# Kernel tuning notes

Measured on AMD Instinct MI355X. Metric: run time of the kernel, lower is better.

The kernel has to match this reference:

```python
import jax, jax.numpy as jnp
import numpy as np

B, S, D_IN, D_OUT = 8, 4096, 512, 64

def setup_inputs() -> dict:
    key = jax.random.key(0)
    k1, k2, k3, k4 = jax.random.split(key, 4)
    scale = 1.0 / np.sqrt(D_IN)
    return {
        "x": jax.random.normal(k1, (B, S, D_IN), dtype=jnp.float32),
        "W_Q": jax.random.normal(k2, (D_IN, D_OUT), dtype=jnp.float32) * scale,
        "W_K": jax.random.normal(k3, (D_IN, D_OUT), dtype=jnp.float32) * scale,
        "W_V": jax.random.normal(k4, (D_IN, D_OUT), dtype=jnp.float32) * scale,
    }

def reference(x, W_Q, W_K, W_V):
    # q,k,v: [B,S,D_OUT]
    q = jnp.einsum("bsd,de->bse", x, W_Q)
    k = jnp.einsum("bsd,de->bse", x, W_K)
    v = jnp.einsum("bsd,de->bse", x, W_V)
    d_out = k.shape[-1]
    # scores: [B,S,S], causal mask (upper triangle -> -inf)
    scores = jnp.einsum("bqe,bke->bqk", q, k)
    s = q.shape[1]
    causal = jnp.tril(jnp.ones((s, s), dtype=bool))
    scores = jnp.where(causal[None, :, :], scores, -jnp.inf)
    attn = jax.nn.softmax(scores / jnp.sqrt(jnp.asarray(d_out, scores.dtype)), axis=-1)
    # dropout p=0.0 (eval) -> identity
    return jnp.einsum("bqk,bke->bqe", attn, v)
```

## Files before the change

kernel.cpp:

```cpp
#include <hip/hip_runtime.h>
#include <hip/hip_bf16.h>

#define B_    8
#define S_    4096
#define DIN   512
#define DOUT  64
#define NROWS (B_ * S_)

typedef __attribute__((ext_vector_type(8)))  short bf16x8;
typedef __attribute__((ext_vector_type(4)))  float f32x4;
typedef __attribute__((ext_vector_type(16))) float f32x16;
typedef __attribute__((ext_vector_type(2)))  unsigned int u32x2;
typedef __attribute__((ext_vector_type(2)))  int i32x2;

typedef const __attribute__((address_space(1))) unsigned int GUI;
typedef __attribute__((address_space(3))) unsigned int LUI;

__device__ __forceinline__ unsigned short f32_to_bf16(float f) {
    union { float f; unsigned int u; } c; c.f = f;
    unsigned int r = (c.u + 0x7FFFu + ((c.u >> 16) & 1u)) >> 16;
    return (unsigned short)r;
}
__device__ __forceinline__ float bf16_to_f32(unsigned short us) {
    union { unsigned int u; float f; } c; c.u = (unsigned int)us << 16;
    return c.f;
}

__device__ __forceinline__ float fast_exp2(float x) {
#if __has_builtin(__builtin_amdgcn_exp2f)
    return __builtin_amdgcn_exp2f(x);
#else
    return exp2f(x);
#endif
}

__device__ __forceinline__ float max_xor32(float v) {
    i32x2 r = __builtin_amdgcn_permlane32_swap(__float_as_int(v), __float_as_int(v),
                                               false, false);
    return fmaxf(__int_as_float(r.x), __int_as_float(r.y));
}
__device__ __forceinline__ float sum_xor32(float v) {
    i32x2 r = __builtin_amdgcn_permlane32_swap(__float_as_int(v), __float_as_int(v),
                                               false, false);
    return __int_as_float(r.x) + __int_as_float(r.y);
}

#define LDS_READS_DONE_FENCE() do {                                   \
    asm volatile("s_waitcnt lgkmcnt(0)" ::: "memory");                \
    __builtin_amdgcn_sched_barrier(0);                                \
} while (0)

__device__ __forceinline__ int pidx_of(int tp, int j) {
    if (tp < 16) return tp - 8;
    if (tp < 24) return 8 + (tp - 16) * 2 + (j - 1);
    return 24 + (tp - 24) * 3 + (j - 1);
}

__global__ void wt_convert(const float* __restrict__ WQ,
                           const float* __restrict__ WK,
                           const float* __restrict__ WV,
                           unsigned short* __restrict__ Wt2) {
    int idx = blockIdx.x * 256 + threadIdx.x;
    if (idx >= 3 * 512 * 16) return;
    int p   = idx / 8192;
    int rem = idx - p * 8192;
    int k   = rem >> 4;
    int n0  = (rem & 15) * 4;
    const float* W = (p == 0) ? WQ : ((p == 1) ? WK : WV);
    float4 v = *(const float4*)(W + k * 64 + n0);
    const int ks = k >> 5, kl = k & 31;
    float vv[4] = {v.x, v.y, v.z, v.w};
#pragma unroll
    for (int r = 0; r < 4; ++r) {
        int n = n0 + r;
        Wt2[(size_t)((ks * 12 + p * 4 + (n >> 4)) * 512) + (n & 15) * 32 + kl] =
            f32_to_bf16(vv[r]);
    }
}

__global__ __launch_bounds__(256) void qkv_proj(const float* __restrict__ x,
                                                const unsigned short* __restrict__ Wt2,
                                                unsigned short* __restrict__ QKV) {
    __shared__ alignas(16) float          xtile[2][1024];
    __shared__ alignas(16) unsigned short btile[2][6144];

    const int tid  = threadIdx.x;
    const int lane = tid & 63;
    const int wq   = tid >> 6;
    const int c15  = lane & 15;
    const int g    = lane >> 4;
    const float* xblk = x + (size_t)blockIdx.x * 32 * DIN;

    const int rw     = (wq & 1) * 16 + c15;
    const int nfbase = (wq >> 1) * 6;

    const int xrow = wq * 8 + (lane >> 3);
    const int xsl  = (lane & 7) ^ (xrow & 7);

    auto stage = [&](int slot, int ks) {
        __builtin_amdgcn_global_load_lds((GUI*)(xblk + ks * 32 + xrow * DIN + xsl * 4),
                                         (LUI*)((char*)&xtile[slot][0] + wq * 1024), 16, 0, 0);
        const unsigned short* Bs = Wt2 + (size_t)ks * 6144;
#pragma unroll
        for (int j = 0; j < 3; ++j)
            __builtin_amdgcn_global_load_lds((GUI*)(Bs + (j * 256 + tid) * 8),
                                             (LUI*)((char*)&btile[slot][0] + j * 4096 + wq * 1024),
                                             16, 0, 0);
    };
    stage(0, 0);
    stage(1, 1);

    f32x4 acc[6] = {};

    int cur = 0;
    for (int ks = 0; ks < 16; ++ks) {
        asm volatile("s_waitcnt vmcnt(4)" ::: "memory");
        asm volatile("s_barrier" ::: "memory");

        const char* xb = (const char*)&xtile[cur][0] + rw * 128;
        f32x4 a0 = *(const f32x4*)(xb + (((2 * g)     ^ (rw & 7)) << 4));
        f32x4 a1 = *(const f32x4*)(xb + (((2 * g + 1) ^ (rw & 7)) << 4));
        union { unsigned w[4]; bf16x8 v; } af;
        asm("v_cvt_pk_bf16_f32 %0, %1, %2" : "=v"(af.w[0]) : "v"(a0[0]), "v"(a0[1]));
        asm("v_cvt_pk_bf16_f32 %0, %1, %2" : "=v"(af.w[1]) : "v"(a0[2]), "v"(a0[3]));
        asm("v_cvt_pk_bf16_f32 %0, %1, %2" : "=v"(af.w[2]) : "v"(a1[0]), "v"(a1[1]));
        asm("v_cvt_pk_bf16_f32 %0, %1, %2" : "=v"(af.w[3]) : "v"(a1[2]), "v"(a1[3]));

        const char* bb = (const char*)&btile[cur][0] + c15 * 64 + g * 16;
#pragma unroll
        for (int n = 0; n < 6; ++n) {
            bf16x8 bf = *(const bf16x8*)(bb + (nfbase + n) * 1024);
            acc[n] = __builtin_amdgcn_mfma_f32_16x16x32_bf16(af.v, bf, acc[n], 0, 0, 0);
        }

        LDS_READS_DONE_FENCE();
        asm volatile("s_barrier" ::: "memory");
        {
            int tn = ks + 2; if (tn > 15) tn = 15;
            stage(cur, tn);
        }
        cur ^= 1;
    }
    asm volatile("s_waitcnt vmcnt(0)" ::: "memory");

    const int orow0 = blockIdx.x * 32 + (wq & 1) * 16 + g * 4;
#pragma unroll
    for (int n = 0; n < 6; ++n) {
        const int nfg  = nfbase + n;
        const int p    = nfg >> 2;
        const int ncol = (nfg & 3) * 16 + c15;
        if (p < 2) {
            unsigned short* outp = QKV + (size_t)p * NROWS * DOUT;
            const float sc = (p == 0) ? 0.125f * 1.44269504089f : 1.0f;
#pragma unroll
            for (int r = 0; r < 4; ++r)
                outp[(size_t)(orow0 + r) * DOUT + ncol] = f32_to_bf16(acc[n][r] * sc);
        } else {
            const int bb2  = orow0 >> 12;
            const int srow = orow0 & 4095;
            union { unsigned short s[4]; u32x2 d; } pk;
#pragma unroll
            for (int r = 0; r < 4; ++r) pk.s[r] = f32_to_bf16(acc[n][r]);
            *(u32x2*)(QKV + (size_t)2 * NROWS * DOUT +
                      ((size_t)bb2 * DOUT + ncol) * S_ + srow) = pk.d;
        }
    }
}

__global__ __launch_bounds__(256) void attn_fwd(const unsigned short* __restrict__ QKV,
                                                float* __restrict__ out,
                                                char* __restrict__ part1,
                                                float* __restrict__ ml0) {
    __shared__ alignas(16) unsigned short k_lds[2][4096];
    __shared__ alignas(16) unsigned short v_lds[2][4096];

    const int bid = blockIdx.x;
    const int b   = bid & 7;
    const int i   = bid >> 3;
    int tp, j;
    if      (i < 8)  { tp = i;                 j = 0; }
    else if (i < 24) { tp = 8 + ((i - 8) >> 1);  j = (i - 8) & 1; }
    else if (i < 48) { tp = 16 + (i - 24) / 3;   j = (i - 24) % 3; }
    else             { tp = 24 + ((i - 48) >> 2); j = (i - 48) & 3; }
    const int qb       = tp * 128;
    const int tile_lo  = 16 * j;
    const int tile_hi  = min(16 * j + 15, 2 * tp + 1);
    const int tile_cnt = tile_hi - tile_lo + 1;

    const int tid  = threadIdx.x;
    const int lane = tid & 63;
    const int wq   = tid >> 6;
    const int q31  = lane & 31;
    const int h    = lane >> 5;
    const int swz  = q31 & 7;
    const int rb0  = q31 * 128;

    const unsigned short* Qg  = QKV + (size_t)b * S_ * DOUT;
    const unsigned short* Kg  = QKV + (size_t)NROWS * DOUT + (size_t)b * S_ * DOUT;
    const unsigned short* VTg = QKV + (size_t)2 * NROWS * DOUT + (size_t)b * DOUT * S_;

    const int qrow = qb + wq * 32 + q31;
    const unsigned short* Qr = Qg + (size_t)qrow * DOUT + 8 * h;
    bf16x8 qf[4];
#pragma unroll
    for (int s = 0; s < 4; ++s) qf[s] = *(const bf16x8*)(Qr + 16 * s);
    asm volatile("s_waitcnt vmcnt(0)" ::: "memory");

    const int i0 = wq * 128 + lane;
    const int i1 = i0 + 64;
    const int r0 = i0 >> 3, s0g = (i0 & 7) ^ (r0 & 7);
    const int r1 = i1 >> 3, s1g = (i1 & 7) ^ (r1 & 7);

    auto stage = [&](int slot, int tg) {
        const unsigned short* Kt = Kg + (size_t)tg * 64 * DOUT;
        const unsigned short* Vt = VTg + tg * 64;
        char* kbase = (char*)&k_lds[slot][0] + wq * 2048;
        char* vbase = (char*)&v_lds[slot][0] + wq * 2048;
        __builtin_amdgcn_global_load_lds((GUI*)(Kt + r0 * DOUT + s0g * 8), (LUI*)kbase, 16, 0, 0);
        __builtin_amdgcn_global_load_lds((GUI*)(Kt + r1 * DOUT + s1g * 8), (LUI*)(kbase + 1024), 16, 0, 0);
        __builtin_amdgcn_global_load_lds((GUI*)(Vt + (size_t)r0 * S_ + s0g * 8), (LUI*)vbase, 16, 0, 0);
        __builtin_amdgcn_global_load_lds((GUI*)(Vt + (size_t)r1 * S_ + s1g * 8), (LUI*)(vbase + 1024), 16, 0, 0);
    };

    stage(0, tile_lo);
    stage(1, tile_lo + (tile_cnt > 1 ? 1 : 0));

    f32x16 oacc0 = {}, oacc1 = {};
    float m_r = -3.0e38f, l_r = 0.f;

    int cur = 0;
    for (int itl = 0; itl < tile_cnt; ++itl) {
        const int tg = tile_lo + itl;
        asm volatile("s_waitcnt vmcnt(4)" ::: "memory");
        asm volatile("s_barrier" ::: "memory");

        const char* kb_ = (const char*)&k_lds[cur][0];
        const char* vb_ = (const char*)&v_lds[cur][0];

        f32x16 sA = {}, sB = {};
#pragma unroll
        for (int s = 0; s < 4; ++s) {
            const int sl = ((2 * s + h) ^ swz) << 4;
            bf16x8 ka  = *(const bf16x8*)(kb_ + rb0 + sl);
            bf16x8 kb2 = *(const bf16x8*)(kb_ + rb0 + 4096 + sl);
            sA = __builtin_amdgcn_mfma_f32_32x32x16_bf16(ka,  qf[s], sA, 0, 0, 0);
            sB = __builtin_amdgcn_mfma_f32_32x32x16_bf16(kb2, qf[s], sB, 0, 0, 0);
        }

        if (tg >= 2 * tp) {
#pragma unroll
            for (int r2 = 0; r2 < 16; ++r2) {
                const int kvg = 64 * tg + (r2 & 3) + 8 * (r2 >> 2) + 4 * h;
                if (kvg      > qrow) sA[r2] = -1.0e30f;
                if (kvg + 32 > qrow) sB[r2] = -1.0e30f;
            }
        }

        float t[16];
#pragma unroll
        for (int k2 = 0; k2 < 16; ++k2) t[k2] = fmaxf(sA[k2], sB[k2]);
#pragma unroll
        for (int st = 8; st >= 1; st >>= 1)
#pragma unroll
            for (int k2 = 0; k2 < st; ++k2) t[k2] = fmaxf(t[k2], t[k2 + st]);
        float mx = max_xor32(t[0]);
        const float mnew  = fmaxf(m_r, mx);
        const float alpha = fast_exp2(m_r - mnew);
        m_r = mnew;

#pragma unroll
        for (int k2 = 0; k2 < 16; ++k2) {
            sA[k2] = fast_exp2(sA[k2] - mnew);
            sB[k2] = fast_exp2(sB[k2] - mnew);
        }
#pragma unroll
        for (int k2 = 0; k2 < 16; ++k2) t[k2] = sA[k2] + sB[k2];
#pragma unroll
        for (int st = 8; st >= 1; st >>= 1)
#pragma unroll
            for (int k2 = 0; k2 < st; ++k2) t[k2] += t[k2 + st];
        l_r = l_r * alpha + sum_xor32(t[0]);

#pragma unroll
        for (int k2 = 0; k2 < 16; ++k2) { oacc0[k2] *= alpha; oacc1[k2] *= alpha; }

#define STEP_PV(u, Pv) do {                                                        \
        const int e0 = 2 * ((u) & 1);                                              \
        unsigned pa, pb2, pc, pd;                                                  \
        asm("v_cvt_pk_bf16_f32 %0, %1, %2" : "=v"(pa)  : "v"(Pv[4*e0+0]), "v"(Pv[4*e0+1])); \
        asm("v_cvt_pk_bf16_f32 %0, %1, %2" : "=v"(pb2) : "v"(Pv[4*e0+2]), "v"(Pv[4*e0+3])); \
        asm("v_cvt_pk_bf16_f32 %0, %1, %2" : "=v"(pc)  : "v"(Pv[4*e0+4]), "v"(Pv[4*e0+5])); \
        asm("v_cvt_pk_bf16_f32 %0, %1, %2" : "=v"(pd)  : "v"(Pv[4*e0+6]), "v"(Pv[4*e0+7])); \
        i32x2 ra = __builtin_amdgcn_permlane32_swap((int)pa,  (int)pc, false, false); \
        i32x2 rb = __builtin_amdgcn_permlane32_swap((int)pb2, (int)pd, false, false); \
        union { unsigned w[4]; bf16x8 v; } pw;                                     \
        pw.w[0] = (unsigned)ra.x; pw.w[1] = (unsigned)rb.x;                        \
        pw.w[2] = (unsigned)ra.y; pw.w[3] = (unsigned)rb.y;                        \
        const int slv = ((2 * (u) + h) ^ swz) << 4;                                \
        bf16x8 vfa = *(const bf16x8*)(vb_ + rb0 + slv);                            \
        bf16x8 vfb = *(const bf16x8*)(vb_ + rb0 + 4096 + slv);                     \
        oacc0 = __builtin_amdgcn_mfma_f32_32x32x16_bf16(vfa, pw.v, oacc0, 0, 0, 0);\
        oacc1 = __builtin_amdgcn_mfma_f32_32x32x16_bf16(vfb, pw.v, oacc1, 0, 0, 0);\
    } while (0)

        STEP_PV(0, sA); STEP_PV(1, sA); STEP_PV(2, sB); STEP_PV(3, sB);
#undef STEP_PV

        LDS_READS_DONE_FENCE();
        asm volatile("s_barrier" ::: "memory");
        {
            int tn = itl + 2; if (tn >= tile_cnt) tn = tile_cnt - 1;
            stage(cur, tile_lo + tn);
        }
        cur ^= 1;
    }

    asm volatile("s_waitcnt vmcnt(0)" ::: "memory");

    const int ql = wq * 32 + q31;
    if (j == 0 && tp < 8) {
        const float linv = 1.0f / l_r;
        float* op = out + (size_t)b * S_ * DOUT + (size_t)qrow * DOUT;
#pragma unroll
        for (int e = 0; e < 4; ++e) {
            f32x4 v0 = { oacc0[4*e+0]*linv, oacc0[4*e+1]*linv, oacc0[4*e+2]*linv, oacc0[4*e+3]*linv };
            f32x4 v1 = { oacc1[4*e+0]*linv, oacc1[4*e+1]*linv, oacc1[4*e+2]*linv, oacc1[4*e+3]*linv };
            *(f32x4*)(op + 8*e + 4*h)      = v0;
            *(f32x4*)(op + 32 + 8*e + 4*h) = v1;
        }
    } else if (j == 0) {
        float* op = out + (size_t)b * S_ * DOUT + (size_t)qrow * DOUT;
#pragma unroll
        for (int e = 0; e < 4; ++e) {
            f32x4 v0 = { oacc0[4*e+0], oacc0[4*e+1], oacc0[4*e+2], oacc0[4*e+3] };
            f32x4 v1 = { oacc1[4*e+0], oacc1[4*e+1], oacc1[4*e+2], oacc1[4*e+3] };
            *(f32x4*)(op + 8*e + 4*h)      = v0;
            *(f32x4*)(op + 32 + 8*e + 4*h) = v1;
        }
        if (h == 0) {
            float* ml = ml0 + (size_t)(b * 24 + (tp - 8)) * 256;
            ml[ql] = m_r; ml[128 + ql] = l_r;
        }
    } else {
        char* pb_ = part1 + (size_t)(b * 48 + pidx_of(tp, j)) * 17408;
        if (h == 0) {
            float* mf = (float*)pb_;
            mf[ql] = m_r; mf[128 + ql] = l_r;
        }
        unsigned short* ob = (unsigned short*)(pb_ + 1024);
#pragma unroll
        for (int e = 0; e < 4; ++e) {
            union { unsigned short s[4]; u32x2 d; } k0, k1;
#pragma unroll
            for (int c = 0; c < 4; ++c) { k0.s[c] = f32_to_bf16(oacc0[4*e+c]);
                                          k1.s[c] = f32_to_bf16(oacc1[4*e+c]); }
            *(u32x2*)(ob + (size_t)ql * 64 + 8*e + 4*h)      = k0.d;
            *(u32x2*)(ob + (size_t)ql * 64 + 32 + 8*e + 4*h) = k1.d;
        }
    }
}

template<int NC>
__device__ __forceinline__ void reduce_body(int b, int tp, int q, int d,
                                            float* __restrict__ out,
                                            const char* __restrict__ part1,
                                            const float* __restrict__ ml0) {
    float* otile = out + ((size_t)b * S_ + (size_t)tp * 128) * 64;
    const float* ml = ml0 + (size_t)(b * 24 + (tp - 8)) * 256;

    float m = ml[q], l = ml[128 + q];
    float M = m;
    float mj[NC - 1], lj[NC - 1];
    const unsigned short* obs[NC - 1];
#pragma unroll
    for (int jj = 0; jj < NC - 1; ++jj) {
        const char* pb = part1 + (size_t)(b * 48 + pidx_of(tp, jj + 1)) * 17408;
        const float* mf = (const float*)pb;
        mj[jj] = mf[q]; lj[jj] = mf[128 + q];
        obs[jj] = (const unsigned short*)(pb + 1024);
        M = fmaxf(M, mj[jj]);
    }
    const float e0 = fast_exp2(m - M);
    float L = e0 * l;
    float O = e0 * otile[(size_t)q * 64 + d];
#pragma unroll
    for (int jj = 0; jj < NC - 1; ++jj) {
        const float ej = fast_exp2(mj[jj] - M);
        L += ej * lj[jj];
        O += ej * bf16_to_f32(obs[jj][(size_t)q * 64 + d]);
    }
    otile[(size_t)q * 64 + d] = O / L;
}

__global__ __launch_bounds__(256) void attn_reduce(float* __restrict__ out,
                                                   const char* __restrict__ part1,
                                                   const float* __restrict__ ml0) {
    const int bid = blockIdx.x;
    const int sub = bid & 31;
    const int tz  = (bid >> 5) % 24;
    const int b   = bid / (32 * 24);
    const int tp  = tz + 8;
    const int q   = sub * 4 + (threadIdx.x >> 6);
    const int d   = threadIdx.x & 63;

    if (tp < 16)      reduce_body<2>(b, tp, q, d, out, part1, ml0);
    else if (tp < 24) reduce_body<3>(b, tp, q, d, out, part1, ml0);
    else              reduce_body<4>(b, tp, q, d, out, part1, ml0);
}

extern "C" void kernel_launch(void* const* d_in, const int* in_sizes, int n_in,
                              void* d_out, int out_size, void* d_ws, size_t ws_size,
                              hipStream_t stream) {
    const float* x  = (const float*)d_in[0];
    const float* WQ = (const float*)d_in[1];
    const float* WK = (const float*)d_in[2];
    const float* WV = (const float*)d_in[3];

    unsigned short* Wt2   = (unsigned short*)d_ws;
    unsigned short* QKV   = Wt2 + 192 * 512;
    char*           part1 = (char*)d_ws + 12779520;
    float*          ml0   = (float*)((char*)d_ws + 19464192);

    wt_convert<<<96, 256, 0, stream>>>(WQ, WK, WV, Wt2);
    qkv_proj<<<1024, 256, 0, stream>>>(x, Wt2, QKV);
    attn_fwd<<<640, 256, 0, stream>>>(QKV, (float*)d_out, part1, ml0);
    attn_reduce<<<6144, 256, 0, stream>>>((float*)d_out, part1, ml0);
}
```

Before: 77.09 us.

## Generalize causal split-KV chunking to templated chunk size and skip idle rescales

Replaces the hardcoded 16-tile split-KV schedule with a templated chunk size computed by a constexpr prefix sum. It launches chunk size 8 when the workspace is large enough, which raises the block count for better CU balance but creates more partials for the reduce pass. It also adds a lazy online-softmax rescale that only updates the running max and rescales accumulators when some lane's new max exceeds the old one by more than a threshold, saving exp and multiply work. The reduce kernel now covers all query tiles, with an early exit for those that need no merging, and uses runtime loops in place of unrolled templates.

```diff
diff --git a/kernel.cpp b/kernel.cpp
--- a/kernel.cpp
+++ b/kernel.cpp
@@ -50,10 +50,10 @@
     __builtin_amdgcn_sched_barrier(0);                                \
 } while (0)
 
-__device__ __forceinline__ int pidx_of(int tp, int j) {
-    if (tp < 16) return tp - 8;
-    if (tp < 24) return 8 + (tp - 16) * 2 + (j - 1);
-    return 24 + (tp - 24) * 3 + (j - 1);
+constexpr int cpbf(int C) {
+    int a = 0;
+    for (int t = 0; t < 32; ++t) a += (2 * t + 2 + C - 1) / C;
+    return a;
 }
 
 __global__ void wt_convert(const float* __restrict__ WQ,
@@ -167,25 +167,31 @@
     }
 }
 
+template<int CHUNK>
 __global__ __launch_bounds__(256) void attn_fwd(const unsigned short* __restrict__ QKV,
                                                 float* __restrict__ out,
                                                 char* __restrict__ part1,
                                                 float* __restrict__ ml0) {
+    constexpr int PPB = cpbf(CHUNK) - 32;
+
     __shared__ alignas(16) unsigned short k_lds[2][4096];
     __shared__ alignas(16) unsigned short v_lds[2][4096];
 
     const int bid = blockIdx.x;
     const int b   = bid & 7;
-    const int i   = bid >> 3;
-    int tp, j;
-    if      (i < 8)  { tp = i;                 j = 0; }
-    else if (i < 24) { tp = 8 + ((i - 8) >> 1);  j = (i - 8) & 1; }
-    else if (i < 48) { tp = 16 + (i - 24) / 3;   j = (i - 24) % 3; }
-    else             { tp = 24 + ((i - 48) >> 2); j = (i - 48) & 3; }
+    const int c   = bid >> 3;
+
+    int tp = 0, acc = 0, nck = 1;
+    for (; tp < 32; ++tp) {
+        nck = (2 * tp + 2 + CHUNK - 1) / CHUNK;
+        if (c < acc + nck) break;
+        acc += nck;
+    }
+    const int j        = c - acc;
+    const int tile_lo  = CHUNK * j;
+    const int tile_hi  = min(CHUNK * j + CHUNK - 1, 2 * tp + 1);
+    const int tile_cnt = tile_hi - tile_lo + 1;
     const int qb       = tp * 128;
-    const int tile_lo  = 16 * j;
-    const int tile_hi  = min(16 * j + 15, 2 * tp + 1);
-    const int tile_cnt = tile_hi - tile_lo + 1;
 
     const int tid  = threadIdx.x;
     const int lane = tid & 63;
@@ -223,7 +229,7 @@
     };
 
     stage(0, tile_lo);
-    stage(1, tile_lo + (tile_cnt > 1 ? 1 : 0));
+    stage(1, tile_lo + 1);
 
     f32x16 oacc0 = {}, oacc1 = {};
     float m_r = -3.0e38f, l_r = 0.f;
@@ -263,15 +269,21 @@
         for (int st = 8; st >= 1; st >>= 1)
 #pragma unroll
             for (int k2 = 0; k2 < st; ++k2) t[k2] = fmaxf(t[k2], t[k2 + st]);
-        float mx = max_xor32(t[0]);
-        const float mnew  = fmaxf(m_r, mx);
-        const float alpha = fast_exp2(m_r - mnew);
-        m_r = mnew;
+        const float mx = max_xor32(t[0]);
+
+        if (__any(mx > m_r + 11.5f)) {
+            const float mnew  = fmaxf(m_r, mx);
+            const float alpha = fast_exp2(m_r - mnew);
+            m_r = mnew;
+            l_r *= alpha;
+#pragma unroll
+            for (int k2 = 0; k2 < 16; ++k2) { oacc0[k2] *= alpha; oacc1[k2] *= alpha; }
+        }
 
 #pragma unroll
         for (int k2 = 0; k2 < 16; ++k2) {
-            sA[k2] = fast_exp2(sA[k2] - mnew);
-            sB[k2] = fast_exp2(sB[k2] - mnew);
+            sA[k2] = fast_exp2(sA[k2] - m_r);
+            sB[k2] = fast_exp2(sB[k2] - m_r);
         }
 #pragma unroll
         for (int k2 = 0; k2 < 16; ++k2) t[k2] = sA[k2] + sB[k2];
@@ -279,10 +291,7 @@
         for (int st = 8; st >= 1; st >>= 1)
 #pragma unroll
             for (int k2 = 0; k2 < st; ++k2) t[k2] += t[k2 + st];
-        l_r = l_r * alpha + sum_xor32(t[0]);
-
-#pragma unroll
-        for (int k2 = 0; k2 < 16; ++k2) { oacc0[k2] *= alpha; oacc1[k2] *= alpha; }
+        l_r += sum_xor32(t[0]);
 
 #define STEP_PV(u, Pv) do {                                                        \
         const int e0 = 2 * ((u) & 1);                                              \
@@ -318,7 +327,7 @@
     asm volatile("s_waitcnt vmcnt(0)" ::: "memory");
 
     const int ql = wq * 32 + q31;
-    if (j == 0 && tp < 8) {
+    if (nck == 1) {
         const float linv = 1.0f / l_r;
         float* op = out + (size_t)b * S_ * DOUT + (size_t)qrow * DOUT;
 #pragma unroll
@@ -338,11 +347,11 @@
             *(f32x4*)(op + 32 + 8*e + 4*h) = v1;
         }
         if (h == 0) {
-            float* ml = ml0 + (size_t)(b * 24 + (tp - 8)) * 256;
+            float* ml = ml0 + (size_t)(b * 32 + tp) * 256;
             ml[ql] = m_r; ml[128 + ql] = l_r;
         }
     } else {
-        char* pb_ = part1 + (size_t)(b * 48 + pidx_of(tp, j)) * 17408;
+        char* pb_ = part1 + (size_t)(b * PPB + (acc - tp) + (j - 1)) * 17408;
         if (h == 0) {
             float* mf = (float*)pb_;
             mf[ql] = m_r; mf[128 + ql] = l_r;
@@ -352,60 +361,53 @@
         for (int e = 0; e < 4; ++e) {
             union { unsigned short s[4]; u32x2 d; } k0, k1;
 #pragma unroll
-            for (int c = 0; c < 4; ++c) { k0.s[c] = f32_to_bf16(oacc0[4*e+c]);
-                                          k1.s[c] = f32_to_bf16(oacc1[4*e+c]); }
+            for (int cc = 0; cc < 4; ++cc) { k0.s[cc] = f32_to_bf16(oacc0[4*e+cc]);
+                                             k1.s[cc] = f32_to_bf16(oacc1[4*e+cc]); }
             *(u32x2*)(ob + (size_t)ql * 64 + 8*e + 4*h)      = k0.d;
             *(u32x2*)(ob + (size_t)ql * 64 + 32 + 8*e + 4*h) = k1.d;
         }
     }
 }
 
-template<int NC>
-__device__ __forceinline__ void reduce_body(int b, int tp, int q, int d,
-                                            float* __restrict__ out,
-                                            const char* __restrict__ part1,
-                                            const float* __restrict__ ml0) {
-    float* otile = out + ((size_t)b * S_ + (size_t)tp * 128) * 64;
-    const float* ml = ml0 + (size_t)(b * 24 + (tp - 8)) * 256;
-
-    float m = ml[q], l = ml[128 + q];
-    float M = m;
-    float mj[NC - 1], lj[NC - 1];
-    const unsigned short* obs[NC - 1];
-#pragma unroll
-    for (int jj = 0; jj < NC - 1; ++jj) {
-        const char* pb = part1 + (size_t)(b * 48 + pidx_of(tp, jj + 1)) * 17408;
-        const float* mf = (const float*)pb;
-        mj[jj] = mf[q]; lj[jj] = mf[128 + q];
-        obs[jj] = (const unsigned short*)(pb + 1024);
-        M = fmaxf(M, mj[jj]);
-    }
-    const float e0 = fast_exp2(m - M);
-    float L = e0 * l;
-    float O = e0 * otile[(size_t)q * 64 + d];
-#pragma unroll
-    for (int jj = 0; jj < NC - 1; ++jj) {
-        const float ej = fast_exp2(mj[jj] - M);
-        L += ej * lj[jj];
-        O += ej * bf16_to_f32(obs[jj][(size_t)q * 64 + d]);
-    }
-    otile[(size_t)q * 64 + d] = O / L;
-}
-
+template<int CHUNK>
 __global__ __launch_bounds__(256) void attn_reduce(float* __restrict__ out,
                                                    const char* __restrict__ part1,
                                                    const float* __restrict__ ml0) {
+    constexpr int PPB = cpbf(CHUNK) - 32;
+
     const int bid = blockIdx.x;
     const int sub = bid & 31;
-    const int tz  = (bid >> 5) % 24;
-    const int b   = bid / (32 * 24);
-    const int tp  = tz + 8;
-    const int q   = sub * 4 + (threadIdx.x >> 6);
-    const int d   = threadIdx.x & 63;
-
-    if (tp < 16)      reduce_body<2>(b, tp, q, d, out, part1, ml0);
-    else if (tp < 24) reduce_body<3>(b, tp, q, d, out, part1, ml0);
-    else              reduce_body<4>(b, tp, q, d, out, part1, ml0);
+    const int tp  = (bid >> 5) & 31;
+    const int b   = bid >> 10;
+
+    const int nck = (2 * tp + 2 + CHUNK - 1) / CHUNK;
+    if (nck < 2) return;
+    int acc = 0;
+    for (int t2 = 0; t2 < tp; ++t2) acc += (2 * t2 + 2 + CHUNK - 1) / CHUNK;
+    const int pbase = acc - tp;
+
+    const int q = sub * 4 + (threadIdx.x >> 6);
+    const int d = threadIdx.x & 63;
+
+    float* otile = out + ((size_t)b * S_ + (size_t)tp * 128) * 64;
+    const float* ml = ml0 + (size_t)(b * 32 + tp) * 256;
+
+    float M = ml[q];
+    for (int jj = 1; jj < nck; ++jj) {
+        const float* mf = (const float*)(part1 + (size_t)(b * PPB + pbase + jj - 1) * 17408);
+        M = fmaxf(M, mf[q]);
+    }
+    const float e0 = fast_exp2(ml[q] - M);
+    float L = e0 * ml[128 + q];
+    float O = e0 * otile[(size_t)q * 64 + d];
+    for (int jj = 1; jj < nck; ++jj) {
+        const char* pb = part1 + (size_t)(b * PPB + pbase + jj - 1) * 17408;
+        const float* mf = (const float*)pb;
+        const float ej = fast_exp2(mf[q] - M);
+        L += ej * mf[128 + q];
+        O += ej * bf16_to_f32(((const unsigned short*)(pb + 1024))[(size_t)q * 64 + d]);
+    }
+    otile[(size_t)q * 64 + d] = O / L;
 }
 
 extern "C" void kernel_launch(void* const* d_in, const int* in_sizes, int n_in,
@@ -419,10 +421,23 @@
     unsigned short* Wt2   = (unsigned short*)d_ws;
     unsigned short* QKV   = Wt2 + 192 * 512;
     char*           part1 = (char*)d_ws + 12779520;
-    float*          ml0   = (float*)((char*)d_ws + 19464192);
+    float* out = (float*)d_out;
 
     wt_convert<<<96, 256, 0, stream>>>(WQ, WK, WV, Wt2);
     qkv_proj<<<1024, 256, 0, stream>>>(x, Wt2, QKV);
-    attn_fwd<<<640, 256, 0, stream>>>(QKV, (float*)d_out, part1, ml0);
-    attn_reduce<<<6144, 256, 0, stream>>>((float*)d_out, part1, ml0);
-}
+
+    constexpr size_t P8  = (size_t)8 * (cpbf(8)  - 32) * 17408;
+    constexpr size_t P16 = (size_t)8 * (cpbf(16) - 32) * 17408;
+    constexpr size_t ML  = (size_t)8 * 32 * 1024;
+    const size_t need8 = 12779520 + P8 + ML;
+
+    if (ws_size >= need8) {
+        float* ml0 = (float*)(part1 + P8);
+        attn_fwd<8><<<8 * cpbf(8), 256, 0, stream>>>(QKV, out, part1, ml0);
+        attn_reduce<8><<<8192, 256, 0, stream>>>(out, part1, ml0);
+    } else {
+        float* ml0 = (float*)(part1 + P16);
+        attn_fwd<16><<<8 * cpbf(16), 256, 0, stream>>>(QKV, out, part1, ml0);
+        attn_reduce<16><<<8192, 256, 0, stream>>>(out, part1, ml0);
+    }
+}
```

After: 87.07 us. 1.13x slower.

## Rework attention to 8 waves of 16x16 MFMA with lazy rescale

Applied to the files above, without the earlier changes.

The attention kernel moves from 4 waves using 32x32x16 MFMAs (32 query rows per wave) to 8 waves using 16x16x32 MFMAs (16 query rows per wave), with 512 threads per block. Probabilities are now sent through a per-wave LDS buffer instead of permlane swaps, and the online-softmax rescale of the accumulators is skipped unless the running max grows by more than a threshold. s_setprio is also raised around the MFMA sections. The aim is more parallelism per CU and less register pressure, at the cost of extra LDS traffic and smaller MFMA shapes.

```diff
diff --git a/kernel.cpp b/kernel.cpp
--- a/kernel.cpp
+++ b/kernel.cpp
@@ -9,7 +9,6 @@
 
 typedef __attribute__((ext_vector_type(8)))  short bf16x8;
 typedef __attribute__((ext_vector_type(4)))  float f32x4;
-typedef __attribute__((ext_vector_type(16))) float f32x16;
 typedef __attribute__((ext_vector_type(2)))  unsigned int u32x2;
 typedef __attribute__((ext_vector_type(2)))  int i32x2;
 
@@ -167,18 +166,19 @@
     }
 }
 
-__global__ __launch_bounds__(256) void attn_fwd(const unsigned short* __restrict__ QKV,
+__global__ __launch_bounds__(512) void attn_fwd(const unsigned short* __restrict__ QKV,
                                                 float* __restrict__ out,
                                                 char* __restrict__ part1,
                                                 float* __restrict__ ml0) {
     __shared__ alignas(16) unsigned short k_lds[2][4096];
     __shared__ alignas(16) unsigned short v_lds[2][4096];
+    __shared__ alignas(16) unsigned short p_lds[8][1024];
 
     const int bid = blockIdx.x;
     const int b   = bid & 7;
     const int i   = bid >> 3;
     int tp, j;
-    if      (i < 8)  { tp = i;                 j = 0; }
+    if      (i < 8)  { tp = i;                   j = 0; }
     else if (i < 24) { tp = 8 + ((i - 8) >> 1);  j = (i - 8) & 1; }
     else if (i < 48) { tp = 16 + (i - 24) / 3;   j = (i - 24) % 3; }
     else             { tp = 24 + ((i - 48) >> 2); j = (i - 48) & 3; }
@@ -190,121 +190,129 @@
     const int tid  = threadIdx.x;
     const int lane = tid & 63;
     const int wq   = tid >> 6;
-    const int q31  = lane & 31;
-    const int h    = lane >> 5;
-    const int swz  = q31 & 7;
-    const int rb0  = q31 * 128;
+    const int c15  = lane & 15;
+    const int g    = lane >> 4;
 
     const unsigned short* Qg  = QKV + (size_t)b * S_ * DOUT;
     const unsigned short* Kg  = QKV + (size_t)NROWS * DOUT + (size_t)b * S_ * DOUT;
     const unsigned short* VTg = QKV + (size_t)2 * NROWS * DOUT + (size_t)b * DOUT * S_;
 
-    const int qrow = qb + wq * 32 + q31;
-    const unsigned short* Qr = Qg + (size_t)qrow * DOUT + 8 * h;
-    bf16x8 qf[4];
-#pragma unroll
-    for (int s = 0; s < 4; ++s) qf[s] = *(const bf16x8*)(Qr + 16 * s);
+    const int ql   = wq * 16 + c15;
+    const int qrow = qb + ql;
+    const size_t qoff = (size_t)qrow * DOUT;
+    bf16x8 qf0 = *(const bf16x8*)(Qg + qoff + g * 8);
+    bf16x8 qf1 = *(const bf16x8*)(Qg + qoff + 32 + g * 8);
     asm volatile("s_waitcnt vmcnt(0)" ::: "memory");
 
-    const int i0 = wq * 128 + lane;
-    const int i1 = i0 + 64;
-    const int r0 = i0 >> 3, s0g = (i0 & 7) ^ (r0 & 7);
-    const int r1 = i1 >> 3, s1g = (i1 & 7) ^ (r1 & 7);
+    const int row = tid >> 3;
+    const int sl  = (tid & 7) ^ (row & 7);
 
     auto stage = [&](int slot, int tg) {
         const unsigned short* Kt = Kg + (size_t)tg * 64 * DOUT;
         const unsigned short* Vt = VTg + tg * 64;
-        char* kbase = (char*)&k_lds[slot][0] + wq * 2048;
-        char* vbase = (char*)&v_lds[slot][0] + wq * 2048;
-        __builtin_amdgcn_global_load_lds((GUI*)(Kt + r0 * DOUT + s0g * 8), (LUI*)kbase, 16, 0, 0);
-        __builtin_amdgcn_global_load_lds((GUI*)(Kt + r1 * DOUT + s1g * 8), (LUI*)(kbase + 1024), 16, 0, 0);
-        __builtin_amdgcn_global_load_lds((GUI*)(Vt + (size_t)r0 * S_ + s0g * 8), (LUI*)vbase, 16, 0, 0);
-        __builtin_amdgcn_global_load_lds((GUI*)(Vt + (size_t)r1 * S_ + s1g * 8), (LUI*)(vbase + 1024), 16, 0, 0);
+        char* kbase = (char*)&k_lds[slot][0] + wq * 1024;
+        char* vbase = (char*)&v_lds[slot][0] + wq * 1024;
+        __builtin_amdgcn_global_load_lds((GUI*)(Kt + row * DOUT + sl * 8), (LUI*)kbase, 16, 0, 0);
+        __builtin_amdgcn_global_load_lds((GUI*)(Vt + (size_t)row * S_ + sl * 8), (LUI*)vbase, 16, 0, 0);
     };
 
     stage(0, tile_lo);
-    stage(1, tile_lo + (tile_cnt > 1 ? 1 : 0));
-
-    f32x16 oacc0 = {}, oacc1 = {};
+    stage(1, tile_lo + 1);
+
+    f32x4 oacc[4] = {};
     float m_r = -3.0e38f, l_r = 0.f;
 
     int cur = 0;
     for (int itl = 0; itl < tile_cnt; ++itl) {
         const int tg = tile_lo + itl;
-        asm volatile("s_waitcnt vmcnt(4)" ::: "memory");
+        asm volatile("s_waitcnt vmcnt(2)" ::: "memory");
         asm volatile("s_barrier" ::: "memory");
 
-        const char* kb_ = (const char*)&k_lds[cur][0];
-        const char* vb_ = (const char*)&v_lds[cur][0];
-
-        f32x16 sA = {}, sB = {};
-#pragma unroll
-        for (int s = 0; s < 4; ++s) {
-            const int sl = ((2 * s + h) ^ swz) << 4;
-            bf16x8 ka  = *(const bf16x8*)(kb_ + rb0 + sl);
-            bf16x8 kb2 = *(const bf16x8*)(kb_ + rb0 + 4096 + sl);
-            sA = __builtin_amdgcn_mfma_f32_32x32x16_bf16(ka,  qf[s], sA, 0, 0, 0);
-            sB = __builtin_amdgcn_mfma_f32_32x32x16_bf16(kb2, qf[s], sB, 0, 0, 0);
-        }
+        const char* kb = (const char*)&k_lds[cur][0];
+        const char* vb = (const char*)&v_lds[cur][0];
+
+        f32x4 s[4];
+        __builtin_amdgcn_s_setprio(1);
+#pragma unroll
+        for (int nf = 0; nf < 4; ++nf) {
+            const char* krow = kb + (nf * 16 + c15) * 128;
+            bf16x8 kf0 = *(const bf16x8*)(krow + ((g ^ (c15 & 7)) << 4));
+            bf16x8 kf1 = *(const bf16x8*)(krow + (((4 + g) ^ (c15 & 7)) << 4));
+            f32x4 z = {};
+            z = __builtin_amdgcn_mfma_f32_16x16x32_bf16(kf0, qf0, z, 0, 0, 0);
+            z = __builtin_amdgcn_mfma_f32_16x16x32_bf16(kf1, qf1, z, 0, 0, 0);
+            s[nf] = z;
+        }
+        __builtin_amdgcn_s_setprio(0);
 
         if (tg >= 2 * tp) {
 #pragma unroll
-            for (int r2 = 0; r2 < 16; ++r2) {
-                const int kvg = 64 * tg + (r2 & 3) + 8 * (r2 >> 2) + 4 * h;
-                if (kvg      > qrow) sA[r2] = -1.0e30f;
-                if (kvg + 32 > qrow) sB[r2] = -1.0e30f;
+            for (int nf = 0; nf < 4; ++nf)
+#pragma unroll
+                for (int r = 0; r < 4; ++r)
+                    if (64 * tg + 16 * nf + 4 * g + r > qrow) s[nf][r] = -1.0e30f;
+        }
+
+        float mx = s[0][0];
+#pragma unroll
+        for (int nf = 0; nf < 4; ++nf)
+#pragma unroll
+            for (int r = 0; r < 4; ++r) mx = fmaxf(mx, s[nf][r]);
+        mx = max_xor32(mx);
+        mx = fmaxf(mx, __shfl_xor(mx, 16, 64));
+
+        if (__any(mx > m_r + 11.5f)) {
+            const float mnew  = fmaxf(m_r, mx);
+            const float alpha = fast_exp2(m_r - mnew);
+            m_r = mnew;
+            l_r *= alpha;
+#pragma unroll
+            for (int df = 0; df < 4; ++df)
+#pragma unroll
+                for (int r = 0; r < 4; ++r) oacc[df][r] *= alpha;
+        }
+
+        float p[4][4];
+        float sum = 0.f;
+#pragma unroll
+        for (int nf = 0; nf < 4; ++nf)
+#pragma unroll
+            for (int r = 0; r < 4; ++r) {
+                p[nf][r] = fast_exp2(s[nf][r] - m_r);
+                sum += p[nf][r];
             }
-        }
-
-        float t[16];
-#pragma unroll
-        for (int k2 = 0; k2 < 16; ++k2) t[k2] = fmaxf(sA[k2], sB[k2]);
-#pragma unroll
-        for (int st = 8; st >= 1; st >>= 1)
-#pragma unroll
-            for (int k2 = 0; k2 < st; ++k2) t[k2] = fmaxf(t[k2], t[k2 + st]);
-        float mx = max_xor32(t[0]);
-        const float mnew  = fmaxf(m_r, mx);
-        const float alpha = fast_exp2(m_r - mnew);
-        m_r = mnew;
-
-#pragma unroll
-        for (int k2 = 0; k2 < 16; ++k2) {
-            sA[k2] = fast_exp2(sA[k2] - mnew);
-            sB[k2] = fast_exp2(sB[k2] - mnew);
-        }
-#pragma unroll
-        for (int k2 = 0; k2 < 16; ++k2) t[k2] = sA[k2] + sB[k2];
-#pragma unroll
-        for (int st = 8; st >= 1; st >>= 1)
-#pragma unroll
-            for (int k2 = 0; k2 < st; ++k2) t[k2] += t[k2 + st];
-        l_r = l_r * alpha + sum_xor32(t[0]);
-
-#pragma unroll
-        for (int k2 = 0; k2 < 16; ++k2) { oacc0[k2] *= alpha; oacc1[k2] *= alpha; }
-
-#define STEP_PV(u, Pv) do {                                                        \
-        const int e0 = 2 * ((u) & 1);                                              \
-        unsigned pa, pb2, pc, pd;                                                  \
-        asm("v_cvt_pk_bf16_f32 %0, %1, %2" : "=v"(pa)  : "v"(Pv[4*e0+0]), "v"(Pv[4*e0+1])); \
-        asm("v_cvt_pk_bf16_f32 %0, %1, %2" : "=v"(pb2) : "v"(Pv[4*e0+2]), "v"(Pv[4*e0+3])); \
-        asm("v_cvt_pk_bf16_f32 %0, %1, %2" : "=v"(pc)  : "v"(Pv[4*e0+4]), "v"(Pv[4*e0+5])); \
-        asm("v_cvt_pk_bf16_f32 %0, %1, %2" : "=v"(pd)  : "v"(Pv[4*e0+6]), "v"(Pv[4*e0+7])); \
-        i32x2 ra = __builtin_amdgcn_permlane32_swap((int)pa,  (int)pc, false, false); \
-        i32x2 rb = __builtin_amdgcn_permlane32_swap((int)pb2, (int)pd, false, false); \
-        union { unsigned w[4]; bf16x8 v; } pw;                                     \
-        pw.w[0] = (unsigned)ra.x; pw.w[1] = (unsigned)rb.x;                        \
-        pw.w[2] = (unsigned)ra.y; pw.w[3] = (unsigned)rb.y;                        \
-        const int slv = ((2 * (u) + h) ^ swz) << 4;                                \
-        bf16x8 vfa = *(const bf16x8*)(vb_ + rb0 + slv);                            \
-        bf16x8 vfb = *(const bf16x8*)(vb_ + rb0 + 4096 + slv);                     \
-        oacc0 = __builtin_amdgcn_mfma_f32_32x32x16_bf16(vfa, pw.v, oacc0, 0, 0, 0);\
-        oacc1 = __builtin_amdgcn_mfma_f32_32x32x16_bf16(vfb, pw.v, oacc1, 0, 0, 0);\
-    } while (0)
-
-        STEP_PV(0, sA); STEP_PV(1, sA); STEP_PV(2, sB); STEP_PV(3, sB);
-#undef STEP_PV
+        sum = sum_xor32(sum);
+        sum += __shfl_xor(sum, 16, 64);
+        l_r += sum;
+
+#pragma unroll
+        for (int nf = 0; nf < 4; ++nf)
+#pragma unroll
+            for (int pr = 0; pr < 2; ++pr) {
+                unsigned pw;
+                asm("v_cvt_pk_bf16_f32 %0, %1, %2"
+                    : "=v"(pw) : "v"(p[nf][2 * pr]), "v"(p[nf][2 * pr + 1]));
+                const int w = 8 * nf + 2 * g + pr;
+                *(unsigned*)((char*)&p_lds[wq][0] + c15 * 128 +
+                             (((w >> 2) ^ (c15 & 7)) << 4) + (w & 3) * 4) = pw;
+            }
+
+        bf16x8 pf[2];
+#pragma unroll
+        for (int kk = 0; kk < 2; ++kk)
+            pf[kk] = *(const bf16x8*)((char*)&p_lds[wq][0] + c15 * 128 +
+                                      (((4 * kk + g) ^ (c15 & 7)) << 4));
+
+        __builtin_amdgcn_s_setprio(1);
+#pragma unroll
+        for (int df = 0; df < 4; ++df) {
+            const char* vrow = vb + (df * 16 + c15) * 128;
+            bf16x8 vf0 = *(const bf16x8*)(vrow + ((g ^ (c15 & 7)) << 4));
+            bf16x8 vf1 = *(const bf16x8*)(vrow + (((4 + g) ^ (c15 & 7)) << 4));
+            oacc[df] = __builtin_amdgcn_mfma_f32_16x16x32_bf16(vf0, pf[0], oacc[df], 0, 0, 0);
+            oacc[df] = __builtin_amdgcn_mfma_f32_16x16x32_bf16(vf1, pf[1], oacc[df], 0, 0, 0);
+        }
+        __builtin_amdgcn_s_setprio(0);
 
         LDS_READS_DONE_FENCE();
         asm volatile("s_barrier" ::: "memory");
@@ -317,45 +325,39 @@
 
     asm volatile("s_waitcnt vmcnt(0)" ::: "memory");
 
-    const int ql = wq * 32 + q31;
     if (j == 0 && tp < 8) {
         const float linv = 1.0f / l_r;
         float* op = out + (size_t)b * S_ * DOUT + (size_t)qrow * DOUT;
 #pragma unroll
-        for (int e = 0; e < 4; ++e) {
-            f32x4 v0 = { oacc0[4*e+0]*linv, oacc0[4*e+1]*linv, oacc0[4*e+2]*linv, oacc0[4*e+3]*linv };
-            f32x4 v1 = { oacc1[4*e+0]*linv, oacc1[4*e+1]*linv, oacc1[4*e+2]*linv, oacc1[4*e+3]*linv };
-            *(f32x4*)(op + 8*e + 4*h)      = v0;
-            *(f32x4*)(op + 32 + 8*e + 4*h) = v1;
+        for (int df = 0; df < 4; ++df) {
+            f32x4 v = { oacc[df][0] * linv, oacc[df][1] * linv,
+                        oacc[df][2] * linv, oacc[df][3] * linv };
+            *(f32x4*)(op + df * 16 + 4 * g) = v;
         }
     } else if (j == 0) {
         float* op = out + (size_t)b * S_ * DOUT + (size_t)qrow * DOUT;
 #pragma unroll
-        for (int e = 0; e < 4; ++e) {
-            f32x4 v0 = { oacc0[4*e+0], oacc0[4*e+1], oacc0[4*e+2], oacc0[4*e+3] };
-            f32x4 v1 = { oacc1[4*e+0], oacc1[4*e+1], oacc1[4*e+2], oacc1[4*e+3] };
-            *(f32x4*)(op + 8*e + 4*h)      = v0;
-            *(f32x4*)(op + 32 + 8*e + 4*h) = v1;
-        }
-        if (h == 0) {
+        for (int df = 0; df < 4; ++df) {
+            f32x4 v = { oacc[df][0], oacc[df][1], oacc[df][2], oacc[df][3] };
+            *(f32x4*)(op + df * 16 + 4 * g) = v;
+        }
+        if (g == 0) {
             float* ml = ml0 + (size_t)(b * 24 + (tp - 8)) * 256;
             ml[ql] = m_r; ml[128 + ql] = l_r;
         }
     } else {
         char* pb_ = part1 + (size_t)(b * 48 + pidx_of(tp, j)) * 17408;
-        if (h == 0) {
+        if (g == 0) {
             float* mf = (float*)pb_;
             mf[ql] = m_r; mf[128 + ql] = l_r;
         }
         unsigned short* ob = (unsigned short*)(pb_ + 1024);
 #pragma unroll
-        for (int e = 0; e < 4; ++e) {
-            union { unsigned short s[4]; u32x2 d; } k0, k1;
-#pragma unroll
-            for (int c = 0; c < 4; ++c) { k0.s[c] = f32_to_bf16(oacc0[4*e+c]);
-                                          k1.s[c] = f32_to_bf16(oacc1[4*e+c]); }
-            *(u32x2*)(ob + (size_t)ql * 64 + 8*e + 4*h)      = k0.d;
-            *(u32x2*)(ob + (size_t)ql * 64 + 32 + 8*e + 4*h) = k1.d;
+        for (int df = 0; df < 4; ++df) {
+            union { unsigned short s2[4]; u32x2 d; } pk;
+#pragma unroll
+            for (int r = 0; r < 4; ++r) pk.s2[r] = f32_to_bf16(oacc[df][r]);
+            *(u32x2*)(ob + (size_t)ql * 64 + df * 16 + 4 * g) = pk.d;
         }
     }
 }
@@ -423,6 +425,6 @@
 
     wt_convert<<<96, 256, 0, stream>>>(WQ, WK, WV, Wt2);
     qkv_proj<<<1024, 256, 0, stream>>>(x, Wt2, QKV);
-    attn_fwd<<<640, 256, 0, stream>>>(QKV, (float*)d_out, part1, ml0);
+    attn_fwd<<<640, 512, 0, stream>>>(QKV, (float*)d_out, part1, ml0);
     attn_reduce<<<6144, 256, 0, stream>>>((float*)d_out, part1, ml0);
 }
```

After: 71.19 us. -7.6%, faster.

## Replace online softmax max with Cauchy-Schwarz bound from Q and K norms

Applied to the files above, without the earlier changes.

Adds two small kernels that compute per-query norms and a running prefix max of per-tile key norms. The attention kernel then uses |q|·max|k| as a fixed softmax offset instead of tracking a running max, which removes the per-tile max reduction, rescaling of the accumulators and the cross-lane max swap. The split-KV reduce no longer needs exponent rescaling, and block order is reversed so the longer tiles launch first. The bound can sit far above the true max, so exp2 values may underflow and lose precision or give a zero denominator on other input distributions, and the two extra launches add overhead.

```diff
diff --git a/kernel.cpp b/kernel.cpp
--- a/kernel.cpp
+++ b/kernel.cpp
@@ -34,11 +34,6 @@
 #endif
 }
 
-__device__ __forceinline__ float max_xor32(float v) {
-    i32x2 r = __builtin_amdgcn_permlane32_swap(__float_as_int(v), __float_as_int(v),
-                                               false, false);
-    return fmaxf(__int_as_float(r.x), __int_as_float(r.y));
-}
 __device__ __forceinline__ float sum_xor32(float v) {
     i32x2 r = __builtin_amdgcn_permlane32_swap(__float_as_int(v), __float_as_int(v),
                                                false, false);
@@ -55,6 +50,8 @@
     if (tp < 24) return 8 + (tp - 16) * 2 + (j - 1);
     return 24 + (tp - 24) * 3 + (j - 1);
 }
+
+#define PART_STRIDE 16896
 
 __global__ void wt_convert(const float* __restrict__ WQ,
                            const float* __restrict__ WK,
@@ -167,7 +164,59 @@
     }
 }
 
+__global__ __launch_bounds__(512) void qk_norms(const unsigned short* __restrict__ QKV,
+                                                float* __restrict__ qn,
+                                                float* __restrict__ ktm) {
+    __shared__ float lds[64];
+    const int bid  = blockIdx.x;
+    const bool isK = bid >= 512;
+    const int blk  = isK ? bid - 512 : bid;
+    const int tid  = threadIdx.x;
+    const int rowl = tid >> 3;
+    const int part = tid & 7;
+    const size_t row = (size_t)blk * 64 + rowl;
+
+    const unsigned short* src = QKV + (isK ? (size_t)NROWS * DOUT : 0) +
+                                row * DOUT + part * 8;
+    bf16x8 v = *(const bf16x8*)src;
+    float s = 0.f;
+#pragma unroll
+    for (int i2 = 0; i2 < 8; ++i2) {
+        float f = bf16_to_f32((unsigned short)v[i2]);
+        s += f * f;
+    }
+    s += __shfl_xor(s, 1, 64);
+    s += __shfl_xor(s, 2, 64);
+    s += __shfl_xor(s, 4, 64);
+
+    if (!isK) {
+        if (part == 0) qn[row] = sqrtf(s);
+    } else {
+        if (part == 0) lds[rowl] = s;
+        __syncthreads();
+        if (tid < 64) {
+            float m = lds[tid];
+#pragma unroll
+            for (int st = 32; st >= 1; st >>= 1)
+                m = fmaxf(m, __shfl_xor(m, st, 64));
+            if (tid == 0) ktm[blk] = sqrtf(m);
+        }
+    }
+}
+
+__global__ void kpref(const float* __restrict__ ktm, float* __restrict__ pm) {
+    const int b = threadIdx.x;
+    if (b >= 8) return;
+    float m = 0.f;
+    for (int t = 0; t < 64; ++t) {
+        m = fmaxf(m, ktm[b * 64 + t]);
+        pm[b * 64 + t] = m;
+    }
+}
+
 __global__ __launch_bounds__(256) void attn_fwd(const unsigned short* __restrict__ QKV,
+                                                const float* __restrict__ qn,
+                                                const float* __restrict__ pm,
                                                 float* __restrict__ out,
                                                 char* __restrict__ part1,
                                                 float* __restrict__ ml0) {
@@ -176,9 +225,9 @@
 
     const int bid = blockIdx.x;
     const int b   = bid & 7;
-    const int i   = bid >> 3;
+    const int i   = 79 - (bid >> 3);
     int tp, j;
-    if      (i < 8)  { tp = i;                 j = 0; }
+    if      (i < 8)  { tp = i;                   j = 0; }
     else if (i < 24) { tp = 8 + ((i - 8) >> 1);  j = (i - 8) & 1; }
     else if (i < 48) { tp = 16 + (i - 24) / 3;   j = (i - 24) % 3; }
     else             { tp = 24 + ((i - 48) >> 2); j = (i - 48) & 3; }
@@ -204,6 +253,8 @@
     bf16x8 qf[4];
 #pragma unroll
     for (int s = 0; s < 4; ++s) qf[s] = *(const bf16x8*)(Qr + 16 * s);
+
+    const float M_r = qn[(size_t)b * S_ + qrow] * pm[b * 64 + (qrow >> 6)];
     asm volatile("s_waitcnt vmcnt(0)" ::: "memory");
 
     const int i0 = wq * 128 + lane;
@@ -223,10 +274,10 @@
     };
 
     stage(0, tile_lo);
-    stage(1, tile_lo + (tile_cnt > 1 ? 1 : 0));
+    stage(1, tile_lo + 1);
 
     f32x16 oacc0 = {}, oacc1 = {};
-    float m_r = -3.0e38f, l_r = 0.f;
+    float l_r = 0.f;
 
     int cur = 0;
     for (int itl = 0; itl < tile_cnt; ++itl) {
@@ -256,33 +307,20 @@
             }
         }
 
-        float t[16];
-#pragma unroll
-        for (int k2 = 0; k2 < 16; ++k2) t[k2] = fmaxf(sA[k2], sB[k2]);
-#pragma unroll
-        for (int st = 8; st >= 1; st >>= 1)
-#pragma unroll
-            for (int k2 = 0; k2 < st; ++k2) t[k2] = fmaxf(t[k2], t[k2 + st]);
-        float mx = max_xor32(t[0]);
-        const float mnew  = fmaxf(m_r, mx);
-        const float alpha = fast_exp2(m_r - mnew);
-        m_r = mnew;
-
+        float t0 = 0.f, t1 = 0.f, t2 = 0.f, t3 = 0.f;
 #pragma unroll
         for (int k2 = 0; k2 < 16; ++k2) {
-            sA[k2] = fast_exp2(sA[k2] - mnew);
-            sB[k2] = fast_exp2(sB[k2] - mnew);
-        }
-#pragma unroll
-        for (int k2 = 0; k2 < 16; ++k2) t[k2] = sA[k2] + sB[k2];
-#pragma unroll
-        for (int st = 8; st >= 1; st >>= 1)
-#pragma unroll
-            for (int k2 = 0; k2 < st; ++k2) t[k2] += t[k2 + st];
-        l_r = l_r * alpha + sum_xor32(t[0]);
-
-#pragma unroll
-        for (int k2 = 0; k2 < 16; ++k2) { oacc0[k2] *= alpha; oacc1[k2] *= alpha; }
+            sA[k2] = fast_exp2(sA[k2] - M_r);
+            sB[k2] = fast_exp2(sB[k2] - M_r);
+        }
+#pragma unroll
+        for (int k2 = 0; k2 < 4; ++k2) {
+            t0 += sA[k2];      t1 += sA[k2 + 4];
+            t0 += sA[k2 + 8];  t1 += sA[k2 + 12];
+            t2 += sB[k2];      t3 += sB[k2 + 4];
+            t2 += sB[k2 + 8];  t3 += sB[k2 + 12];
+        }
+        l_r += (t0 + t1) + (t2 + t3);
 
 #define STEP_PV(u, Pv) do {                                                        \
         const int e0 = 2 * ((u) & 1);                                              \
@@ -317,6 +355,8 @@
 
     asm volatile("s_waitcnt vmcnt(0)" ::: "memory");
 
+    l_r = sum_xor32(l_r);
+
     const int ql = wq * 32 + q31;
     if (j == 0 && tp < 8) {
         const float linv = 1.0f / l_r;
@@ -337,17 +377,11 @@
             *(f32x4*)(op + 8*e + 4*h)      = v0;
             *(f32x4*)(op + 32 + 8*e + 4*h) = v1;
         }
-        if (h == 0) {
-            float* ml = ml0 + (size_t)(b * 24 + (tp - 8)) * 256;
-            ml[ql] = m_r; ml[128 + ql] = l_r;
-        }
+        if (h == 0) ml0[(size_t)(b * 24 + (tp - 8)) * 128 + ql] = l_r;
     } else {
-        char* pb_ = part1 + (size_t)(b * 48 + pidx_of(tp, j)) * 17408;
-        if (h == 0) {
-            float* mf = (float*)pb_;
-            mf[ql] = m_r; mf[128 + ql] = l_r;
-        }
-        unsigned short* ob = (unsigned short*)(pb_ + 1024);
+        char* pb_ = part1 + (size_t)(b * 48 + pidx_of(tp, j)) * PART_STRIDE;
+        if (h == 0) ((float*)pb_)[ql] = l_r;
+        unsigned short* ob = (unsigned short*)(pb_ + 512);
 #pragma unroll
         for (int e = 0; e < 4; ++e) {
             union { unsigned short s[4]; u32x2 d; } k0, k1;
@@ -366,28 +400,13 @@
                                             const char* __restrict__ part1,
                                             const float* __restrict__ ml0) {
     float* otile = out + ((size_t)b * S_ + (size_t)tp * 128) * 64;
-    const float* ml = ml0 + (size_t)(b * 24 + (tp - 8)) * 256;
-
-    float m = ml[q], l = ml[128 + q];
-    float M = m;
-    float mj[NC - 1], lj[NC - 1];
-    const unsigned short* obs[NC - 1];
+    float L = ml0[(size_t)(b * 24 + (tp - 8)) * 128 + q];
+    float O = otile[(size_t)q * 64 + d];
 #pragma unroll
     for (int jj = 0; jj < NC - 1; ++jj) {
-        const char* pb = part1 + (size_t)(b * 48 + pidx_of(tp, jj + 1)) * 17408;
-        const float* mf = (const float*)pb;
-        mj[jj] = mf[q]; lj[jj] = mf[128 + q];
-        obs[jj] = (const unsigned short*)(pb + 1024);
-        M = fmaxf(M, mj[jj]);
-    }
-    const float e0 = fast_exp2(m - M);
-    float L = e0 * l;
-    float O = e0 * otile[(size_t)q * 64 + d];
-#pragma unroll
-    for (int jj = 0; jj < NC - 1; ++jj) {
-        const float ej = fast_exp2(mj[jj] - M);
-        L += ej * lj[jj];
-        O += ej * bf16_to_f32(obs[jj][(size_t)q * 64 + d]);
+        const char* pb = part1 + (size_t)(b * 48 + pidx_of(tp, jj + 1)) * PART_STRIDE;
+        L += ((const float*)pb)[q];
+        O += bf16_to_f32(((const unsigned short*)(pb + 512))[(size_t)q * 64 + d]);
     }
     otile[(size_t)q * 64 + d] = O / L;
 }
@@ -419,10 +438,16 @@
     unsigned short* Wt2   = (unsigned short*)d_ws;
     unsigned short* QKV   = Wt2 + 192 * 512;
     char*           part1 = (char*)d_ws + 12779520;
-    float*          ml0   = (float*)((char*)d_ws + 19464192);
+    float*          ml0   = (float*)((char*)d_ws + 19267584);
+    float*          qn    = (float*)((char*)d_ws + 19365888);
+    float*          ktm   = (float*)((char*)d_ws + 19496960);
+    float*          pmb   = (float*)((char*)d_ws + 19499008);
+    float* out = (float*)d_out;
 
     wt_convert<<<96, 256, 0, stream>>>(WQ, WK, WV, Wt2);
     qkv_proj<<<1024, 256, 0, stream>>>(x, Wt2, QKV);
-    attn_fwd<<<640, 256, 0, stream>>>(QKV, (float*)d_out, part1, ml0);
-    attn_reduce<<<6144, 256, 0, stream>>>((float*)d_out, part1, ml0);
-}
+    qk_norms<<<1024, 512, 0, stream>>>(QKV, qn, ktm);
+    kpref<<<1, 64, 0, stream>>>(ktm, pmb);
+    attn_fwd<<<640, 256, 0, stream>>>(QKV, qn, pmb, out, part1, ml0);
+    attn_reduce<<<6144, 256, 0, stream>>>(out, part1, ml0);
+}
```

After: 78.24 us. No clear change (+1.5%).
